# Kernel tuning notes

Hardware: AMD Instinct MI355X
Metric: run time of the kernel (lower is better)

## Reference

```python
import jax, jax.numpy as jnp
import numpy as np

EPS = 1e-5


def conv3x3(x, w):
    # x: [B,C,H,W], w: [O,I,3,3], stride 1, pad 1 (torch Conv2d bias=False)
    return jax.lax.conv_general_dilated(
        x, w, window_strides=(1, 1), padding=((1, 1), (1, 1)),
        dimension_numbers=("NCHW", "OIHW", "NCHW"))


def batchnorm(y, g, b, m, v):
    # inference-style BN with running stats
    s = (g * jax.lax.rsqrt(v + EPS)).reshape(1, -1, 1, 1)
    t = (b - m * g * jax.lax.rsqrt(v + EPS)).reshape(1, -1, 1, 1)
    return y * s + t


def setup_inputs() -> dict:
    key = jax.random.key(0)
    ks = jax.random.split(key, 12)
    bs, c, h, w, T = 32, 64, 96, 96, 64
    inp = {}
    inp["x"] = jax.random.normal(ks[0], (bs, c, h, w), jnp.float32)
    inp["ref_x"] = jax.random.normal(ks[1], (bs, c, 1, 1), jnp.float32)
    inp["ref_types"] = jax.random.randint(ks[2], (bs,), 0, T, jnp.int32)
    # feat_extract: two BasicConv2d (conv3x3 no bias + BN + ReLU)
    inp["conv1_w"] = jax.random.normal(ks[3], (c, c, 3, 3), jnp.float32) * 0.05
    inp["bn1_g"] = jnp.ones((c,), jnp.float32)
    inp["bn1_b"] = jnp.zeros((c,), jnp.float32)
    inp["bn1_m"] = jnp.zeros((c,), jnp.float32)
    inp["bn1_v"] = jnp.ones((c,), jnp.float32)
    inp["conv2_w"] = jax.random.normal(ks[4], (c, c, 3, 3), jnp.float32) * 0.05
    inp["bn2_g"] = jnp.ones((c,), jnp.float32)
    inp["bn2_b"] = jnp.zeros((c,), jnp.float32)
    inp["bn2_m"] = jnp.zeros((c,), jnp.float32)
    inp["bn2_v"] = jnp.ones((c,), jnp.float32)
    # weight_mlp: Linear(c, 2c) -> ReLU -> Linear(2c, T)
    inp["mlp_w1"] = jax.random.normal(ks[5], (c, 2 * c), jnp.float32) * 0.05
    inp["mlp_b1"] = jnp.zeros((2 * c,), jnp.float32)
    inp["mlp_w2"] = jax.random.normal(ks[6], (2 * c, T), jnp.float32) * 0.05
    inp["mlp_b2"] = jnp.zeros((T,), jnp.float32)
    # reference buffer (torch registers zeros; use small randn so output is nontrivial)
    inp["ref_proj"] = jax.random.normal(ks[7], (T, c), jnp.float32) * 0.05
    return inp


def reference(x, ref_x, ref_types, conv1_w, bn1_g, bn1_b, bn1_m, bn1_v,
              conv2_w, bn2_g, bn2_b, bn2_m, bn2_v,
              mlp_w1, mlp_b1, mlp_w2, mlp_b2, ref_proj):
    momentum = jnp.float32(0.99)
    temperature = jnp.float32(1.0)
    bs, c, h, w = x.shape
    T = ref_proj.shape[0]

    # feat_extract + global average pool
    f = jax.nn.relu(batchnorm(conv3x3(x, conv1_w), bn1_g, bn1_b, bn1_m, bn1_v))
    f = jax.nn.relu(batchnorm(conv3x3(f, conv2_w), bn2_g, bn2_b, bn2_m, bn2_v))
    x_feat = f.mean(axis=(2, 3))  # [bs, c]

    # weight MLP -> tempered softmax
    type_logits = jax.nn.relu(x_feat @ mlp_w1 + mlp_b1) @ mlp_w2 + mlp_b2  # [bs, T]
    type_weights = jax.nn.softmax(type_logits / temperature, axis=1)

    # sequential per-sample EMA scatter, vectorized in closed form:
    # ref_new[t] = m^{k_t} * ref_proj[t] + sum_i 1[type_i=t] (1-m) m^{#later occ of t} v_i
    ref_vec = ref_x.reshape(bs, c)
    onehot = jax.nn.one_hot(ref_types, T, dtype=x.dtype)        # [bs, T]
    counts = onehot.sum(axis=0)                                  # [T]
    occ_after = counts[None, :] - jnp.cumsum(onehot, axis=0)     # strictly-after count
    w_i = (1.0 - momentum) * (momentum ** occ_after) * onehot    # [bs, T]
    ref_new = (momentum ** counts)[:, None] * ref_proj + w_i.T @ ref_vec  # [T, c]

    # weighted reference from (updated) buffer
    weighted_ref = (type_weights @ ref_new).reshape(bs, c, 1, 1)
    out = weighted_ref + ref_x

    # supervision loss: cross entropy (mean)
    logp = jax.nn.log_softmax(type_logits, axis=1)
    loss = -jnp.take_along_axis(logp, ref_types[:, None].astype(jnp.int32), axis=1).mean()
    return out, loss, ref_new
```

## Files before the change

kernel.cpp:

```cpp
#include <hip/hip_runtime.h>
#include <math.h>

#define BATCH 32
#define CH    64
#define HH    96
#define WW    96
#define NT    64

using short8 = __attribute__((ext_vector_type(8))) short;
using f32x16 = __attribute__((ext_vector_type(16))) float;

#define WS_XFS   0
#define WS_ZERO  8192
#define WS_A1    8448
#define WS_A2    82176
#define WS_XT    155904
#define WS_F1T   37904640

__device__ __forceinline__ unsigned short b16(float f) {
    unsigned int u = __builtin_bit_cast(unsigned int, f);
    unsigned int r = (u + 0x7FFFu + ((u >> 16) & 1u)) >> 16;
    return (unsigned short)r;
}

__device__ __forceinline__ void gl_lds16(const void* g, void* l) {
    __builtin_amdgcn_global_load_lds(
        (const __attribute__((address_space(1))) unsigned int*)g,
        (__attribute__((address_space(3))) unsigned int*)l, 16, 0, 0);
}

__global__ void prep_small(const float* __restrict__ c1w, const float* __restrict__ c2w,
                           char* __restrict__ ws) {
    const int bid = blockIdx.x, tx = threadIdx.x;
    if (bid < 288) {
        const float* w = bid < 144 ? c1w : c2w;
        unsigned short* At = (unsigned short*)(ws + (bid < 144 ? WS_A1 : WS_A2));
        int idx = (bid % 144) * 256 + tx;
        int j = idx & 7, g1 = idx >> 3;
        int ga = g1 % 576, mc = g1 / 576;
        int c = mc & 3, mt = mc >> 1 >> 1;
        int tap = ga >> 6, kb = (ga >> 5) & 1, ol = ga & 31;
        int o = mt * 32 + ol, ci = c * 16 + kb * 8 + j;
        At[idx] = b16(w[(o * 64 + ci) * 9 + tap]);
    } else {
        int i = (bid - 288) * 256 + tx;
        if (i < 2112) ((float*)ws)[i] = 0.f;
    }
}

__global__ __launch_bounds__(256)
void prep_x(const float* __restrict__ x, unsigned short* __restrict__ xt) {
    int gid = blockIdx.x * 256 + threadIdx.x;
    int cig = gid / 294912;
    int p   = gid % 294912;
    int b   = p / 9216;
    int hw  = p % 9216;
    const float* src = x + (size_t)(b * 64 + cig * 8) * 9216 + hw;
    ushort4 lo, hi;
    lo.x = b16(src[0 * 9216]); lo.y = b16(src[1 * 9216]);
    lo.z = b16(src[2 * 9216]); lo.w = b16(src[3 * 9216]);
    hi.x = b16(src[4 * 9216]); hi.y = b16(src[5 * 9216]);
    hi.z = b16(src[6 * 9216]); hi.w = b16(src[7 * 9216]);
    ushort4* dst = (ushort4*)(xt + (size_t)p * 64 + cig * 8);
    dst[0] = lo; dst[1] = hi;
}

template <int POOL>
__global__ __launch_bounds__(256, 4)
void conv_mfma(const unsigned short* __restrict__ xt, const unsigned short* __restrict__ Aprep,
               const unsigned short* __restrict__ zerop,
               const float* __restrict__ gg, const float* __restrict__ bb,
               const float* __restrict__ mm, const float* __restrict__ vv_,
               unsigned short* __restrict__ f1t, float* __restrict__ xfs) {
    __shared__ char smem[28160];
    float* s_s = (float*)(smem + 27648);
    float* s_t = (float*)(smem + 27904);

    const int tx = threadIdx.x;
    const int rg = blockIdx.x;
    const int b  = blockIdx.y;
    const int mt = blockIdx.z;
    const int r0 = rg * 4;
    const int wv = tx >> 6, l = tx & 63;
    const int rh = wv;
    const int kb = l >> 5, ln = l & 31;

    if (tx < 64) {
        float inv = rsqrtf(vv_[tx] + 1e-5f);
        s_s[tx] = gg[tx] * inv;
        s_t[tx] = bb[tx] - mm[tx] * gg[tx] * inv;
    }

    const char* srcp0; const char* srcp1; const char* srcp2; const char* srcp3; const char* srcp4;
    {
        const char* sp[5];
#pragma unroll
        for (int i = 0; i < 5; ++i) {
            int g  = i * 256 + tx;
            int lg = g ^ ((g >> 3) & 7);
            int row = lg / 192, s = lg % 192;
            int col = s >> 1, kb2 = s & 1;
            int grow = r0 - 1 + row;
            if (grow >= 0 && grow < 96)
                sp[i] = (const char*)(xt + ((size_t)(b * 96 + grow) * 96 + col) * 64 + kb2 * 8);
            else
                sp[i] = (const char*)zerop;
        }
        srcp0 = sp[0]; srcp1 = sp[1]; srcp2 = sp[2]; srcp3 = sp[3]; srcp4 = sp[4];
    }
    const char* abase = (const char*)Aprep + mt * 36864 + (size_t)tx * 16;

    int boff[3][3];
#pragma unroll
    for (int nt = 0; nt < 3; ++nt)
#pragma unroll
        for (int dw = 0; dw < 3; ++dw) {
            int cc = nt * 32 + ln + dw - 1;
            int ccc = cc < 0 ? 0 : (cc > 95 ? 95 : cc);
            int s = ccc * 2 + kb;
            boff[nt][dw] = rh * 3072 + (s ^ ((s >> 3) & 7)) * 16;
        }
    const bool msk0 = (ln == 0), msk2 = (ln == 31);

    f32x16 acc[3] = {};

    for (int c = 0; c < 4; ++c) {
        __syncthreads();
        gl_lds16(srcp0 + c * 32, smem + 0     + wv * 1024);
        gl_lds16(srcp1 + c * 32, smem + 4096  + wv * 1024);
        gl_lds16(srcp2 + c * 32, smem + 8192  + wv * 1024);
        gl_lds16(srcp3 + c * 32, smem + 12288 + wv * 1024);
        if (tx < 128)
            gl_lds16(srcp4 + c * 32, smem + 16384 + wv * 1024);
        gl_lds16(abase + c * 9216,        smem + 18432 + wv * 1024);
        gl_lds16(abase + c * 9216 + 4096, smem + 22528 + wv * 1024);
        if (tx < 64)
            gl_lds16(abase + c * 9216 + 8192, smem + 26624 + wv * 1024);
        __syncthreads();

#pragma unroll
        for (int tap = 0; tap < 9; ++tap) {
            const int dh = tap / 3, dw = tap % 3;
            short8 af = *(const short8*)(smem + 18432 + tap * 1024 + kb * 512 + ln * 16);
#pragma unroll
            for (int nt = 0; nt < 3; ++nt) {
                short8 bf = *(const short8*)(smem + dh * 3072 + boff[nt][dw]);
                if (nt == 0 && dw == 0) bf = msk0 ? (short8){} : bf;
                if (nt == 2 && dw == 2) bf = msk2 ? (short8){} : bf;
                acc[nt] = __builtin_amdgcn_mfma_f32_32x32x16_bf16(af, bf, acc[nt], 0, 0, 0);
            }
        }
    }

    if (POOL == 0) {
        unsigned short* orow = f1t + (size_t)((b * 96 + r0 + rh) * 96) * 64;
#pragma unroll
        for (int nt = 0; nt < 3; ++nt) {
            const int col = nt * 32 + ln;
#pragma unroll
            for (int qh = 0; qh < 4; ++qh) {
                const int ob = 8 * qh + 4 * kb;
                uint2 pk;
                float y0 = fmaxf(fmaf(acc[nt][qh * 4 + 0], s_s[mt * 32 + ob + 0], s_t[mt * 32 + ob + 0]), 0.f);
                float y1 = fmaxf(fmaf(acc[nt][qh * 4 + 1], s_s[mt * 32 + ob + 1], s_t[mt * 32 + ob + 1]), 0.f);
                float y2 = fmaxf(fmaf(acc[nt][qh * 4 + 2], s_s[mt * 32 + ob + 2], s_t[mt * 32 + ob + 2]), 0.f);
                float y3 = fmaxf(fmaf(acc[nt][qh * 4 + 3], s_s[mt * 32 + ob + 3], s_t[mt * 32 + ob + 3]), 0.f);
                pk.x = (unsigned)b16(y0) | ((unsigned)b16(y1) << 16);
                pk.y = (unsigned)b16(y2) | ((unsigned)b16(y3) << 16);
                *(uint2*)(orow + (size_t)col * 64 + mt * 32 + ob) = pk;
            }
        }
    } else {
#pragma unroll
        for (int qh = 0; qh < 4; ++qh)
#pragma unroll
            for (int j = 0; j < 4; ++j) {
                const int o = mt * 32 + 8 * qh + 4 * kb + j;
                const float ss = s_s[o], tt = s_t[o];
                float y = fmaxf(fmaf(acc[0][qh * 4 + j], ss, tt), 0.f)
                        + fmaxf(fmaf(acc[1][qh * 4 + j], ss, tt), 0.f)
                        + fmaxf(fmaf(acc[2][qh * 4 + j], ss, tt), 0.f);
#pragma unroll
                for (int off = 1; off < 32; off <<= 1) y += __shfl_xor(y, off, 64);
                if (ln == 0) atomicAdd(&xfs[b * 64 + o], y);
            }
    }
}

__global__ __launch_bounds__(1024)
void head_kernel(const float* __restrict__ xfs, const float* __restrict__ rx,
                 const int* __restrict__ ty_g,
                 const float* __restrict__ w1, const float* __restrict__ b1,
                 const float* __restrict__ w2, const float* __restrict__ b2,
                 const float* __restrict__ rproj, float* __restrict__ out) {
    __shared__ float xf[BATCH][64];
    __shared__ float hb[BATCH][128];
    __shared__ float lg[BATCH][NT];
    __shared__ float rnew[NT][64];
    __shared__ float rxs[BATCH * 64];
    __shared__ int   ty[BATCH];
    __shared__ float lossb[BATCH];

    const int tx = threadIdx.x;

    for (int i = tx; i < BATCH * 64; i += 1024) {
        xf[i >> 6][i & 63] = xfs[i] * (1.f / 9216.f);
        rxs[i] = rx[i];
    }
    if (tx < BATCH) ty[tx] = ty_g[tx];
    __syncthreads();

    {
        int idx = tx;
#pragma unroll
        for (int u = 0; u < 4; ++u, idx += 1024) {
            int bb_ = idx >> 7, j = idx & 127;
            float s = b1[j];
#pragma unroll 8
            for (int c = 0; c < 64; ++c) s = fmaf(xf[bb_][c], w1[c * 128 + j], s);
            hb[bb_][j] = fmaxf(s, 0.f);
        }
    }
    __syncthreads();

    {
        int idx = tx;
#pragma unroll
        for (int u = 0; u < 2; ++u, idx += 1024) {
            int bb_ = idx >> 6, t = idx & 63;
            float s = b2[t];
#pragma unroll 8
            for (int j = 0; j < 128; ++j) s = fmaf(hb[bb_][j], w2[j * 64 + t], s);
            lg[bb_][t] = s;
        }
    }
    __syncthreads();

    float (*tw)[NT] = (float (*)[NT])xf;
    if (tx < BATCH) {
        int b = tx;
        float mx = -1e30f;
        for (int t = 0; t < NT; ++t) mx = fmaxf(mx, lg[b][t]);
        float sum = 0.f;
        for (int t = 0; t < NT; ++t) sum += expf(lg[b][t] - mx);
        float inv = 1.f / sum;
        for (int t = 0; t < NT; ++t) tw[b][t] = expf(lg[b][t] - mx) * inv;
        lossb[b] = -(lg[b][ty[b]] - mx - logf(sum));
    }
    __syncthreads();

    for (int idx = tx; idx < NT * 64; idx += 1024) {
        int t = idx >> 6, c = idx & 63;
        float r = rproj[idx];
#pragma unroll 8
        for (int i = 0; i < BATCH; ++i)
            if (ty[i] == t) r = 0.99f * r + 0.01f * rxs[i * 64 + c];
        rnew[t][c] = r;
        out[2049 + idx] = r;
    }
    __syncthreads();

    for (int idx = tx; idx < BATCH * 64; idx += 1024) {
        int b = idx >> 6, c = idx & 63;
        float s = 0.f;
#pragma unroll 8
        for (int t = 0; t < NT; ++t) s = fmaf(tw[b][t], rnew[t][c], s);
        out[idx] = s + rxs[idx];
    }
    if (tx == 0) {
        float s = 0.f;
        for (int b = 0; b < BATCH; ++b) s += lossb[b];
        out[2048] = s * (1.f / 32.f);
    }
}

extern "C" void kernel_launch(void* const* d_in, const int* in_sizes, int n_in,
                              void* d_out, int out_size, void* d_ws, size_t ws_size,
                              hipStream_t stream) {
    const float* x    = (const float*)d_in[0];
    const float* rx   = (const float*)d_in[1];
    const int*   ty   = (const int*)d_in[2];
    const float* c1w  = (const float*)d_in[3];
    const float* bn1g = (const float*)d_in[4];
    const float* bn1b = (const float*)d_in[5];
    const float* bn1m = (const float*)d_in[6];
    const float* bn1v = (const float*)d_in[7];
    const float* c2w  = (const float*)d_in[8];
    const float* bn2g = (const float*)d_in[9];
    const float* bn2b = (const float*)d_in[10];
    const float* bn2m = (const float*)d_in[11];
    const float* bn2v = (const float*)d_in[12];
    const float* w1   = (const float*)d_in[13];
    const float* b1   = (const float*)d_in[14];
    const float* w2   = (const float*)d_in[15];
    const float* b2   = (const float*)d_in[16];
    const float* rpj  = (const float*)d_in[17];

    char* ws = (char*)d_ws;
    float*          xfs = (float*)(ws + WS_XFS);
    unsigned short* zp  = (unsigned short*)(ws + WS_ZERO);
    unsigned short* A1  = (unsigned short*)(ws + WS_A1);
    unsigned short* A2  = (unsigned short*)(ws + WS_A2);
    unsigned short* x_t = (unsigned short*)(ws + WS_XT);
    unsigned short* f1t = (unsigned short*)(ws + WS_F1T);
    float*          out = (float*)d_out;

    prep_small<<<297, 256, 0, stream>>>(c1w, c2w, ws);
    prep_x<<<9216, 256, 0, stream>>>(x, x_t);

    dim3 grid(24, 32, 2);
    conv_mfma<0><<<grid, 256, 0, stream>>>(x_t, A1, zp, bn1g, bn1b, bn1m, bn1v, f1t, nullptr);
    conv_mfma<1><<<grid, 256, 0, stream>>>(f1t, A2, zp, bn2g, bn2b, bn2m, bn2v, nullptr, xfs);

    head_kernel<<<1, 1024, 0, stream>>>(xfs, rx, ty, w1, b1, w2, b2, rpj, out);
}
```

Measured before the change: 339.5 us.

## Compute both output-channel tiles per block and use channel-planar bf16 layout

```diff
diff --git a/kernel.cpp b/kernel.cpp
--- a/kernel.cpp
+++ b/kernel.cpp
@@ -16,6 +16,7 @@
 #define WS_A2    82176
 #define WS_XT    155904
 #define WS_F1T   37904640
+#define PLANE    9437184
 
 __device__ __forceinline__ unsigned short b16(float f) {
     unsigned int u = __builtin_bit_cast(unsigned int, f);
@@ -38,7 +39,7 @@
         int idx = (bid % 144) * 256 + tx;
         int j = idx & 7, g1 = idx >> 3;
         int ga = g1 % 576, mc = g1 / 576;
-        int c = mc & 3, mt = mc >> 1 >> 1;
+        int c = mc & 3, mt = mc >> 2;
         int tap = ga >> 6, kb = (ga >> 5) & 1, ol = ga & 31;
         int o = mt * 32 + ol, ci = c * 16 + kb * 8 + j;
         At[idx] = b16(w[(o * 64 + ci) * 9 + tap]);
@@ -49,38 +50,47 @@
 }
 
 __global__ __launch_bounds__(256)
-void prep_x(const float* __restrict__ x, unsigned short* __restrict__ xt) {
+void prep_x(const float* __restrict__ x, char* __restrict__ xt) {
     int gid = blockIdx.x * 256 + threadIdx.x;
-    int cig = gid / 294912;
-    int p   = gid % 294912;
+    int cig = gid / 147456;
+    int pp  = gid % 147456;
+    int p   = pp * 2;
     int b   = p / 9216;
     int hw  = p % 9216;
     const float* src = x + (size_t)(b * 64 + cig * 8) * 9216 + hw;
-    ushort4 lo, hi;
-    lo.x = b16(src[0 * 9216]); lo.y = b16(src[1 * 9216]);
-    lo.z = b16(src[2 * 9216]); lo.w = b16(src[3 * 9216]);
-    hi.x = b16(src[4 * 9216]); hi.y = b16(src[5 * 9216]);
-    hi.z = b16(src[6 * 9216]); hi.w = b16(src[7 * 9216]);
-    ushort4* dst = (ushort4*)(xt + (size_t)p * 64 + cig * 8);
-    dst[0] = lo; dst[1] = hi;
+    float2 v0 = *(const float2*)(src + 0 * 9216);
+    float2 v1 = *(const float2*)(src + 1 * 9216);
+    float2 v2 = *(const float2*)(src + 2 * 9216);
+    float2 v3 = *(const float2*)(src + 3 * 9216);
+    float2 v4 = *(const float2*)(src + 4 * 9216);
+    float2 v5 = *(const float2*)(src + 5 * 9216);
+    float2 v6 = *(const float2*)(src + 6 * 9216);
+    float2 v7 = *(const float2*)(src + 7 * 9216);
+    int c = cig >> 1, kb2 = cig & 1;
+    char* dst = xt + (size_t)c * PLANE + (size_t)p * 32 + kb2 * 16;
+    ushort4 a0, a1, c0, c1;
+    a0.x = b16(v0.x); a0.y = b16(v1.x); a0.z = b16(v2.x); a0.w = b16(v3.x);
+    a1.x = b16(v4.x); a1.y = b16(v5.x); a1.z = b16(v6.x); a1.w = b16(v7.x);
+    c0.x = b16(v0.y); c0.y = b16(v1.y); c0.z = b16(v2.y); c0.w = b16(v3.y);
+    c1.x = b16(v4.y); c1.y = b16(v5.y); c1.z = b16(v6.y); c1.w = b16(v7.y);
+    *(ushort4*)(dst)      = a0; *(ushort4*)(dst + 8)  = a1;
+    *(ushort4*)(dst + 32) = c0; *(ushort4*)(dst + 40) = c1;
 }
 
 template <int POOL>
-__global__ __launch_bounds__(256, 4)
-void conv_mfma(const unsigned short* __restrict__ xt, const unsigned short* __restrict__ Aprep,
-               const unsigned short* __restrict__ zerop,
+__global__ __launch_bounds__(512, 2)
+void conv_mfma(const char* __restrict__ xt, const char* __restrict__ Aprep,
+               const char* __restrict__ zerop,
                const float* __restrict__ gg, const float* __restrict__ bb,
                const float* __restrict__ mm, const float* __restrict__ vv_,
-               unsigned short* __restrict__ f1t, float* __restrict__ xfs) {
-    __shared__ char smem[28160];
-    float* s_s = (float*)(smem + 27648);
-    float* s_t = (float*)(smem + 27904);
+               char* __restrict__ f1t, float* __restrict__ xfs) {
+    __shared__ char smem[31232];
+    float* s_s = (float*)(smem + 30720);
+    float* s_t = s_s + 64;
 
     const int tx = threadIdx.x;
-    const int rg = blockIdx.x;
+    const int r0 = blockIdx.x * 8;
     const int b  = blockIdx.y;
-    const int mt = blockIdx.z;
-    const int r0 = rg * 4;
     const int wv = tx >> 6, l = tx & 63;
     const int rh = wv;
     const int kb = l >> 5, ln = l & 31;
@@ -91,99 +101,105 @@
         s_t[tx] = bb[tx] - mm[tx] * gg[tx] * inv;
     }
 
-    const char* srcp0; const char* srcp1; const char* srcp2; const char* srcp3; const char* srcp4;
-    {
-        const char* sp[5];
-#pragma unroll
-        for (int i = 0; i < 5; ++i) {
-            int g  = i * 256 + tx;
-            int lg = g ^ ((g >> 3) & 7);
-            int row = lg / 192, s = lg % 192;
-            int col = s >> 1, kb2 = s & 1;
-            int grow = r0 - 1 + row;
-            if (grow >= 0 && grow < 96)
-                sp[i] = (const char*)(xt + ((size_t)(b * 96 + grow) * 96 + col) * 64 + kb2 * 8);
-            else
-                sp[i] = (const char*)zerop;
-        }
-        srcp0 = sp[0]; srcp1 = sp[1]; srcp2 = sp[2]; srcp3 = sp[3]; srcp4 = sp[4];
-    }
-    const char* abase = (const char*)Aprep + mt * 36864 + (size_t)tx * 16;
-
-    int boff[3][3];
+    const char* sin[4];
+    bool oob[4];
+#pragma unroll
+    for (int i = 0; i < 4; ++i) {
+        int q = wv + 8 * i;
+        int g = q * 64 + l;
+        int row = g / 192, t = g % 192;
+        int kb2 = t / 96, col = t % 96;
+        int grow = r0 - 1 + row;
+        oob[i] = (grow < 0) || (grow >= 96);
+        int gr = oob[i] ? 0 : grow;
+        sin[i] = xt + (size_t)((b * 96 + gr) * 96 + col) * 32 + kb2 * 16;
+    }
+    const char* abase = Aprep + (kb * 32 + ln) * 16;
+
+    int bcol[3][3];
 #pragma unroll
     for (int nt = 0; nt < 3; ++nt)
 #pragma unroll
         for (int dw = 0; dw < 3; ++dw) {
             int cc = nt * 32 + ln + dw - 1;
             int ccc = cc < 0 ? 0 : (cc > 95 ? 95 : cc);
-            int s = ccc * 2 + kb;
-            boff[nt][dw] = rh * 3072 + (s ^ ((s >> 3) & 7)) * 16;
+            bcol[nt][dw] = kb * 1536 + ccc * 16;
         }
     const bool msk0 = (ln == 0), msk2 = (ln == 31);
 
-    f32x16 acc[3] = {};
-
+    f32x16 acc[2][3] = {};
+
+#pragma unroll
     for (int c = 0; c < 4; ++c) {
         __syncthreads();
-        gl_lds16(srcp0 + c * 32, smem + 0     + wv * 1024);
-        gl_lds16(srcp1 + c * 32, smem + 4096  + wv * 1024);
-        gl_lds16(srcp2 + c * 32, smem + 8192  + wv * 1024);
-        gl_lds16(srcp3 + c * 32, smem + 12288 + wv * 1024);
-        if (tx < 128)
-            gl_lds16(srcp4 + c * 32, smem + 16384 + wv * 1024);
-        gl_lds16(abase + c * 9216,        smem + 18432 + wv * 1024);
-        gl_lds16(abase + c * 9216 + 4096, smem + 22528 + wv * 1024);
-        if (tx < 64)
-            gl_lds16(abase + c * 9216 + 8192, smem + 26624 + wv * 1024);
+#pragma unroll
+        for (int i = 0; i < 4; ++i) {
+            int q = wv + 8 * i;
+            if (q < 30) {
+                const char* s = oob[i] ? zerop : (sin[i] + (size_t)c * PLANE);
+                gl_lds16(s, smem + q * 1024);
+            }
+        }
+        short8 af[2][9];
+#pragma unroll
+        for (int mt = 0; mt < 2; ++mt)
+#pragma unroll
+            for (int tap = 0; tap < 9; ++tap)
+                af[mt][tap] = *(const short8*)(abase + mt * 36864 + c * 9216 + tap * 1024);
         __syncthreads();
 
+        const char* brow = smem + rh * 3072;
 #pragma unroll
         for (int tap = 0; tap < 9; ++tap) {
             const int dh = tap / 3, dw = tap % 3;
-            short8 af = *(const short8*)(smem + 18432 + tap * 1024 + kb * 512 + ln * 16);
 #pragma unroll
             for (int nt = 0; nt < 3; ++nt) {
-                short8 bf = *(const short8*)(smem + dh * 3072 + boff[nt][dw]);
+                short8 bf = *(const short8*)(brow + dh * 3072 + bcol[nt][dw]);
                 if (nt == 0 && dw == 0) bf = msk0 ? (short8){} : bf;
                 if (nt == 2 && dw == 2) bf = msk2 ? (short8){} : bf;
-                acc[nt] = __builtin_amdgcn_mfma_f32_32x32x16_bf16(af, bf, acc[nt], 0, 0, 0);
+                acc[0][nt] = __builtin_amdgcn_mfma_f32_32x32x16_bf16(af[0][tap], bf, acc[0][nt], 0, 0, 0);
+                acc[1][nt] = __builtin_amdgcn_mfma_f32_32x32x16_bf16(af[1][tap], bf, acc[1][nt], 0, 0, 0);
             }
         }
     }
 
+    const int r = r0 + rh;
     if (POOL == 0) {
-        unsigned short* orow = f1t + (size_t)((b * 96 + r0 + rh) * 96) * 64;
 #pragma unroll
         for (int nt = 0; nt < 3; ++nt) {
-            const int col = nt * 32 + ln;
-#pragma unroll
-            for (int qh = 0; qh < 4; ++qh) {
-                const int ob = 8 * qh + 4 * kb;
-                uint2 pk;
-                float y0 = fmaxf(fmaf(acc[nt][qh * 4 + 0], s_s[mt * 32 + ob + 0], s_t[mt * 32 + ob + 0]), 0.f);
-                float y1 = fmaxf(fmaf(acc[nt][qh * 4 + 1], s_s[mt * 32 + ob + 1], s_t[mt * 32 + ob + 1]), 0.f);
-                float y2 = fmaxf(fmaf(acc[nt][qh * 4 + 2], s_s[mt * 32 + ob + 2], s_t[mt * 32 + ob + 2]), 0.f);
-                float y3 = fmaxf(fmaf(acc[nt][qh * 4 + 3], s_s[mt * 32 + ob + 3], s_t[mt * 32 + ob + 3]), 0.f);
-                pk.x = (unsigned)b16(y0) | ((unsigned)b16(y1) << 16);
-                pk.y = (unsigned)b16(y2) | ((unsigned)b16(y3) << 16);
-                *(uint2*)(orow + (size_t)col * 64 + mt * 32 + ob) = pk;
-            }
+            int p = (b * 96 + r) * 96 + nt * 32 + ln;
+            char* pb = f1t + (size_t)p * 32 + kb * 8;
+#pragma unroll
+            for (int mt = 0; mt < 2; ++mt)
+#pragma unroll
+                for (int qh = 0; qh < 4; ++qh) {
+                    const int ob = mt * 32 + 8 * qh + 4 * kb;
+                    float y0 = fmaxf(fmaf(acc[mt][nt][qh * 4 + 0], s_s[ob + 0], s_t[ob + 0]), 0.f);
+                    float y1 = fmaxf(fmaf(acc[mt][nt][qh * 4 + 1], s_s[ob + 1], s_t[ob + 1]), 0.f);
+                    float y2 = fmaxf(fmaf(acc[mt][nt][qh * 4 + 2], s_s[ob + 2], s_t[ob + 2]), 0.f);
+                    float y3 = fmaxf(fmaf(acc[mt][nt][qh * 4 + 3], s_s[ob + 3], s_t[ob + 3]), 0.f);
+                    uint2 pk;
+                    pk.x = (unsigned)b16(y0) | ((unsigned)b16(y1) << 16);
+                    pk.y = (unsigned)b16(y2) | ((unsigned)b16(y3) << 16);
+                    *(uint2*)(pb + (size_t)(mt * 2 + (qh >> 1)) * PLANE + (qh & 1) * 16) = pk;
+                }
         }
     } else {
 #pragma unroll
-        for (int qh = 0; qh < 4; ++qh)
-#pragma unroll
-            for (int j = 0; j < 4; ++j) {
-                const int o = mt * 32 + 8 * qh + 4 * kb + j;
-                const float ss = s_s[o], tt = s_t[o];
-                float y = fmaxf(fmaf(acc[0][qh * 4 + j], ss, tt), 0.f)
-                        + fmaxf(fmaf(acc[1][qh * 4 + j], ss, tt), 0.f)
-                        + fmaxf(fmaf(acc[2][qh * 4 + j], ss, tt), 0.f);
-#pragma unroll
-                for (int off = 1; off < 32; off <<= 1) y += __shfl_xor(y, off, 64);
-                if (ln == 0) atomicAdd(&xfs[b * 64 + o], y);
-            }
+        for (int mt = 0; mt < 2; ++mt)
+#pragma unroll
+            for (int qh = 0; qh < 4; ++qh)
+#pragma unroll
+                for (int j = 0; j < 4; ++j) {
+                    const int o = mt * 32 + 8 * qh + 4 * kb + j;
+                    const float ss = s_s[o], tt = s_t[o];
+                    float y = fmaxf(fmaf(acc[mt][0][qh * 4 + j], ss, tt), 0.f)
+                            + fmaxf(fmaf(acc[mt][1][qh * 4 + j], ss, tt), 0.f)
+                            + fmaxf(fmaf(acc[mt][2][qh * 4 + j], ss, tt), 0.f);
+#pragma unroll
+                    for (int off = 1; off < 32; off <<= 1) y += __shfl_xor(y, off, 64);
+                    if (ln == 0) atomicAdd(&xfs[b * 64 + o], y);
+                }
     }
 }
 
@@ -297,20 +313,20 @@
     const float* rpj  = (const float*)d_in[17];
 
     char* ws = (char*)d_ws;
-    float*          xfs = (float*)(ws + WS_XFS);
-    unsigned short* zp  = (unsigned short*)(ws + WS_ZERO);
-    unsigned short* A1  = (unsigned short*)(ws + WS_A1);
-    unsigned short* A2  = (unsigned short*)(ws + WS_A2);
-    unsigned short* x_t = (unsigned short*)(ws + WS_XT);
-    unsigned short* f1t = (unsigned short*)(ws + WS_F1T);
-    float*          out = (float*)d_out;
+    float* xfs = (float*)(ws + WS_XFS);
+    char*  zp  = ws + WS_ZERO;
+    char*  A1  = ws + WS_A1;
+    char*  A2  = ws + WS_A2;
+    char*  x_t = ws + WS_XT;
+    char*  f1t = ws + WS_F1T;
+    float* out = (float*)d_out;
 
     prep_small<<<297, 256, 0, stream>>>(c1w, c2w, ws);
-    prep_x<<<9216, 256, 0, stream>>>(x, x_t);
-
-    dim3 grid(24, 32, 2);
-    conv_mfma<0><<<grid, 256, 0, stream>>>(x_t, A1, zp, bn1g, bn1b, bn1m, bn1v, f1t, nullptr);
-    conv_mfma<1><<<grid, 256, 0, stream>>>(f1t, A2, zp, bn2g, bn2b, bn2m, bn2v, nullptr, xfs);
+    prep_x<<<4608, 256, 0, stream>>>(x, x_t);
+
+    dim3 grid(12, 32);
+    conv_mfma<0><<<grid, 512, 0, stream>>>(x_t, A1, zp, bn1g, bn1b, bn1m, bn1v, f1t, nullptr);
+    conv_mfma<1><<<grid, 512, 0, stream>>>(f1t, A2, zp, bn2g, bn2b, bn2m, bn2v, nullptr, xfs);
 
     head_kernel<<<1, 1024, 0, stream>>>(xfs, rx, ty, w1, b1, w2, b2, rpj, out);
 }
```

After: 305.2 us. 10.1% less time.
